# Performance work log

Measured on AMD Instinct MI355X. Metric: run time of the kernel, lower is better.

The kernel has to match this reference:

```python
import jax, jax.numpy as jnp
import numpy as np

NUM_BUSES = 20000
NUM_LINES = 320000
OTHER = 1000
BATCH = 128


def setup_inputs() -> dict:
    key = jax.random.key(0)
    k1, k2, k3, k4, k5 = jax.random.split(key, 5)
    x = jax.random.normal(k1, (BATCH, 2 * NUM_BUSES + OTHER), dtype=jnp.float32)
    from_indices = jax.random.randint(k2, (NUM_LINES,), 0, NUM_BUSES, dtype=jnp.int32)
    to_indices = jax.random.randint(k3, (NUM_LINES,), 0, NUM_BUSES, dtype=jnp.int32)
    # reactances bounded away from 0 (realistic p.u. line reactances)
    reactances = 0.01 + 0.2 * jax.random.uniform(k4, (NUM_LINES,), dtype=jnp.float32)
    limits = 0.5 + 1.5 * jax.random.uniform(k5, (NUM_LINES,), dtype=jnp.float32)
    return {
        "x": x,
        "from_indices": from_indices,
        "to_indices": to_indices,
        "reactances": reactances,
        "limits": limits,
        "num_buses": NUM_BUSES,
    }


def reference(x, from_indices, to_indices, reactances, limits, num_buses):
    nb = num_buses
    voltages = x[:, :nb]                     # [B, nb]
    angles = x[:, nb:2 * nb]                 # [B, nb]
    other_params = x[:, 2 * nb:]             # [B, other]

    from_a = angles[:, from_indices]         # [B, L] gather
    to_a = angles[:, to_indices]
    angle_diffs = from_a - to_a
    flows = angle_diffs / reactances[None, :]
    over = jnp.abs(flows / limits[None, :]) > 1.0

    # Torch runs this branch only if any line is over limit; when none are,
    # adjustments are identically zero, so applying unconditionally is exact.
    required = jnp.sign(angle_diffs) * (reactances * limits)[None, :]
    adjustments = jnp.where(over, required, angle_diffs) - angle_diffs  # [B, L]
    half = adjustments * 0.5
    # angles = angles + from_adjustments - to_adjustments
    #        = angles + scatter_add(from, adj/2) + scatter_add(to, adj/2)
    # (torch accumulates -adj/2 into to_adjustments, then subtracts it)
    delta = jnp.zeros_like(angles).at[:, from_indices].add(half).at[:, to_indices].add(half)
    angles2 = angles + delta

    diffs2 = angles2[:, from_indices] - angles2[:, to_indices]
    flows2 = diffs2 / reactances[None, :]

    out = jnp.concatenate([voltages, angles2, other_params], axis=1)
    return out, flows2
```

## Files before the change

kernel.cpp:

```cpp
#include <hip/hip_runtime.h>

#define NB     20000
#define NL     320000
#define NOTH   1000
#define BATCH  128
#define ROW    (2*NB + NOTH)
#define CAP    80
#define NBLK   256
#define LSEG   (NL/NBLK)
#define BCHUNK 8
#define CB     (NB/BCHUNK)
#define NSLICE 2
#define LPS    (NL/NSLICE)

__device__ __forceinline__ float fast_rcp(float a)
{
    float r;
    asm volatile("v_rcp_f32 %0, %1" : "=v"(r) : "v"(a));
    return r;
}

__global__ __launch_bounds__(512) void histo_k(
    const int* __restrict__ fidx, const int* __restrict__ tidx,
    ushort* __restrict__ H)
{
    extern __shared__ uint h[];
    for (int i = threadIdx.x; i < NB; i += 512) h[i] = 0u;
    __syncthreads();

    const int l0 = blockIdx.x * LSEG;
    for (int l = l0 + (int)threadIdx.x; l < l0 + LSEG; l += 512) {
        atomicAdd(&h[fidx[l]], 1u);
        atomicAdd(&h[tidx[l]], 1u);
    }
    __syncthreads();

    ushort* __restrict__ Hrow = H + (size_t)blockIdx.x * NB;
    for (int i = threadIdx.x; i < NB / 2; i += 512) {
        ushort2 u; u.x = (ushort)h[2 * i]; u.y = (ushort)h[2 * i + 1];
        ((ushort2*)Hrow)[i] = u;
    }
}

__global__ __launch_bounds__(512) void scan_k(
    ushort* __restrict__ H, int* __restrict__ cnt)
{
    const int u = blockIdx.x * 512 + threadIdx.x;
    if (u >= NB) return;
    uint run = 0;
    for (int b = 0; b < NBLK; ++b) {
        const uint v = H[(size_t)b * NB + u];
        H[(size_t)b * NB + u] = (ushort)run;
        run += v;
    }
    cnt[u] = (int)run;
}

__global__ __launch_bounds__(512) void place_k(
    const int* __restrict__ fidx, const int* __restrict__ tidx,
    const float* __restrict__ xr, const float* __restrict__ lim,
    const ushort* __restrict__ H, unsigned* __restrict__ bins)
{
    extern __shared__ char sm[];
    uint*   __restrict__ h    = (uint*)sm;
    ushort* __restrict__ pref = (ushort*)(sm + NB * 4);

    const ushort* __restrict__ Hrow = H + (size_t)blockIdx.x * NB;
    for (int i = threadIdx.x; i < NB; i += 512) h[i] = 0u;
    for (int i = threadIdx.x; i < NB / 2; i += 512)
        ((ushort2*)pref)[i] = ((const ushort2*)Hrow)[i];
    __syncthreads();

    const int l0 = blockIdx.x * LSEG;
    for (int l = l0 + (int)threadIdx.x; l < l0 + LSEG; l += 512) {
        const int fi = fidx[l];
        const int ti = tidx[l];
        union { float f; unsigned u; } c; c.f = xr[l] * lim[l];
        const unsigned rl16 = (c.u + 0x8000u) >> 16;

        const uint s0 = (uint)pref[fi] + atomicAdd(&h[fi], 1u);
        if (s0 < CAP) bins[(size_t)s0 * NB + fi] = ((unsigned)ti << 17) | rl16;
        const uint s1 = (uint)pref[ti] + atomicAdd(&h[ti], 1u);
        if (s1 < CAP) bins[(size_t)s1 * NB + ti] =
            ((unsigned)fi << 17) | (1u << 16) | rl16;
    }
}

__global__ __launch_bounds__(256) void zero_k(int* __restrict__ cnt)
{
    const int i = blockIdx.x * 256 + threadIdx.x;
    if (i < NB / 4) ((int4*)cnt)[i] = make_int4(0, 0, 0, 0);
}

__global__ __launch_bounds__(256) void build_k(
    const int* __restrict__ fidx, const int* __restrict__ tidx,
    const float* __restrict__ xr, const float* __restrict__ lim,
    int* __restrict__ cnt, unsigned* __restrict__ bins)
{
    const int q = blockIdx.x * 256 + threadIdx.x;
    if (q >= NL / 4) return;
    const int4   f = ((const int4*)fidx)[q];
    const int4   t = ((const int4*)tidx)[q];
    const float4 r = ((const float4*)xr)[q];
    const float4 L = ((const float4*)lim)[q];
    #define EMIT(FI, TI, RC, LC)                                             \
    {                                                                        \
        union { float f; unsigned u; } c; c.f = (RC) * (LC);                 \
        const unsigned rl16 = (c.u + 0x8000u) >> 16;                         \
        const int p0 = atomicAdd(&cnt[FI], 1);                               \
        if (p0 < CAP) bins[(size_t)p0 * NB + (FI)] =                         \
            ((unsigned)(TI) << 17) | rl16;                                   \
        const int p1 = atomicAdd(&cnt[TI], 1);                               \
        if (p1 < CAP) bins[(size_t)p1 * NB + (TI)] =                         \
            ((unsigned)(FI) << 17) | (1u << 16) | rl16;                      \
    }
    EMIT(f.x, t.x, r.x, L.x)
    EMIT(f.y, t.y, r.y, L.y)
    EMIT(f.z, t.z, r.z, L.z)
    EMIT(f.w, t.w, r.w, L.w)
    #undef EMIT
}

__global__ __launch_bounds__(1024) void delta_copy_k(
    const float* __restrict__ x, const int* __restrict__ cnt,
    const unsigned* __restrict__ bins, float* __restrict__ out)
{
    extern __shared__ float a[];
    const int b  = blockIdx.x % BATCH;
    const int cb = blockIdx.x / BATCH;

    const float* __restrict__ xrow = x   + (size_t)b * ROW;
    float*       __restrict__ orow = out + (size_t)b * ROW;

    for (int i = threadIdx.x; i < NB / 4; i += 1024)
        ((float4*)a)[i] = ((const float4*)(xrow + NB))[i];
    __syncthreads();

    for (int i = threadIdx.x; i < CB / 4; i += 1024)
        ((float4*)(orow + cb * CB))[i] = ((const float4*)(xrow + cb * CB))[i];
    if (cb == 0)
        for (int i = threadIdx.x; i < NOTH / 4; i += 1024)
            ((float4*)(orow + 2 * NB))[i] = ((const float4*)(xrow + 2 * NB))[i];

    const int base = cb * CB;
    for (int bus = base + (int)threadIdx.x; bus < base + CB; bus += 1024) {
        const int   n  = min(cnt[bus], CAP);
        const float ab = a[bus];
        float ds = 0.0f;
        int k = 0;
        #define CONTRIB(W)                                                   \
        {                                                                    \
            const unsigned w  = (W);                                         \
            const int   other = (int)(w >> 17);                              \
            const float rl    = __uint_as_float((w & 0xFFFFu) << 16);        \
            const float ad    = ab - a[other];                               \
            if (fabsf(ad) > rl) {                                            \
                float hh = 0.5f * (copysignf(rl, ad) - ad);                  \
                if (w & (1u << 16)) hh = -hh;                                \
                ds += hh;                                                    \
            }                                                                \
        }
        for (; k + 4 <= n; k += 4) {
            const unsigned w0 = bins[(size_t)(k + 0) * NB + bus];
            const unsigned w1 = bins[(size_t)(k + 1) * NB + bus];
            const unsigned w2 = bins[(size_t)(k + 2) * NB + bus];
            const unsigned w3 = bins[(size_t)(k + 3) * NB + bus];
            CONTRIB(w0) CONTRIB(w1) CONTRIB(w2) CONTRIB(w3)
        }
        for (; k < n; ++k) CONTRIB(bins[(size_t)k * NB + bus])
        #undef CONTRIB
        orow[NB + bus] = ab + ds;
    }
}

__global__ __launch_bounds__(1024) void flows_lds_k(
    const float* __restrict__ out, const int* __restrict__ fidx,
    const int* __restrict__ tidx, const float* __restrict__ xr,
    float* __restrict__ f2)
{
    extern __shared__ float a2[];
    const int b = blockIdx.x % BATCH;
    const int s = blockIdx.x / BATCH;

    const float* __restrict__ src = out + (size_t)b * ROW + NB;
    for (int i = threadIdx.x; i < NB / 4; i += 1024)
        ((float4*)a2)[i] = ((const float4*)src)[i];
    __syncthreads();

    float* __restrict__ frow = f2 + (size_t)b * NL;
    const int q0 = s * (LPS / 4);
    const int q1 = q0 + (LPS / 4);
    for (int q = q0 + (int)threadIdx.x; q < q1; q += 1024) {
        const int4   f = ((const int4*)fidx)[q];
        const int4   t = ((const int4*)tidx)[q];
        const float4 r = ((const float4*)xr)[q];
        float4 o;
        o.x = (a2[f.x] - a2[t.x]) * fast_rcp(r.x);
        o.y = (a2[f.y] - a2[t.y]) * fast_rcp(r.y);
        o.z = (a2[f.z] - a2[t.z]) * fast_rcp(r.z);
        o.w = (a2[f.w] - a2[t.w]) * fast_rcp(r.w);
        ((float4*)frow)[q] = o;
    }
}

extern "C" void kernel_launch(void* const* d_in, const int* in_sizes, int n_in,
                              void* d_out, int out_size, void* d_ws, size_t ws_size,
                              hipStream_t stream)
{
    const float* x   = (const float*)d_in[0];
    const int*   fi  = (const int*)  d_in[1];
    const int*   ti  = (const int*)  d_in[2];
    const float* xr  = (const float*)d_in[3];
    const float* lim = (const float*)d_in[4];

    float* out    = (float*)d_out;
    float* flows2 = out + (size_t)BATCH * ROW;

    const size_t hBytes = (size_t)NBLK * NB * sizeof(ushort);
    const size_t needed = hBytes + (size_t)NB * 4 + (size_t)CAP * NB * 4;

    int* cnt;
    unsigned* bins;

    if (ws_size >= needed) {
        ushort* H = (ushort*)d_ws;
        cnt  = (int*)((char*)d_ws + hBytes);
        bins = (unsigned*)((char*)d_ws + hBytes + (size_t)NB * 4);

        histo_k<<<dim3(NBLK), dim3(512), NB * sizeof(uint), stream>>>(fi, ti, H);
        scan_k<<<dim3((NB + 511) / 512), dim3(512), 0, stream>>>(H, cnt);
        place_k<<<dim3(NBLK), dim3(512),
                  NB * sizeof(uint) + NB * sizeof(ushort), stream>>>(
            fi, ti, xr, lim, H, bins);
    } else {
        cnt  = (int*)d_ws;
        bins = (unsigned*)((char*)d_ws + (size_t)NB * 4);
        zero_k<<<dim3((NB / 4 + 255) / 256), dim3(256), 0, stream>>>(cnt);
        build_k<<<dim3((NL / 4 + 255) / 256), dim3(256), 0, stream>>>(
            fi, ti, xr, lim, cnt, bins);
    }

    delta_copy_k<<<dim3(BCHUNK * BATCH), dim3(1024), NB * sizeof(float), stream>>>(
        x, cnt, bins, out);

    flows_lds_k<<<dim3(NSLICE * BATCH), dim3(1024), NB * sizeof(float), stream>>>(
        out, fi, ti, xr, flows2);
}
```

Baseline: 116.2 us.

## Overlap passthrough copy with scan, slice flows more, use nontemporal stores

Moves the voltage and other-params passthrough copy out of the delta kernel into extra blocks of the scan kernel. The scan uses only 40 blocks, so the idle CUs can do the copy alongside it. The flows kernel is split into 4 slices per batch row instead of 2 and writes its output with nontemporal stores. The workspace-size fallback path is removed, so the code now assumes the workspace is always large enough. Splitting into more slices means more blocks each reload the angle row into LDS.

```diff
diff --git a/kernel.cpp b/kernel.cpp
--- a/kernel.cpp
+++ b/kernel.cpp
@@ -10,8 +10,14 @@
 #define LSEG   (NL/NBLK)
 #define BCHUNK 8
 #define CB     (NB/BCHUNK)
-#define NSLICE 2
+#define NSLICE 4
 #define LPS    (NL/NSLICE)
+
+#define SCANB  40
+#define COPYB  256
+#define CPF4   (BATCH*(NB/4 + NOTH/4))
+
+typedef float vf4 __attribute__((ext_vector_type(4)));
 
 __device__ __forceinline__ float fast_rcp(float a)
 {
@@ -42,18 +48,31 @@
     }
 }
 
-__global__ __launch_bounds__(512) void scan_k(
-    ushort* __restrict__ H, int* __restrict__ cnt)
-{
-    const int u = blockIdx.x * 512 + threadIdx.x;
-    if (u >= NB) return;
-    uint run = 0;
-    for (int b = 0; b < NBLK; ++b) {
-        const uint v = H[(size_t)b * NB + u];
-        H[(size_t)b * NB + u] = (ushort)run;
-        run += v;
-    }
-    cnt[u] = (int)run;
+__global__ __launch_bounds__(512) void scancopy_k(
+    ushort* __restrict__ H, int* __restrict__ cnt,
+    const float* __restrict__ x, float* __restrict__ out)
+{
+    if (blockIdx.x < SCANB) {
+        const int u = blockIdx.x * 512 + threadIdx.x;
+        if (u >= NB) return;
+        uint run = 0;
+        for (int b = 0; b < NBLK; ++b) {
+            const uint v = H[(size_t)b * NB + u];
+            H[(size_t)b * NB + u] = (ushort)run;
+            run += v;
+        }
+        cnt[u] = (int)run;
+    } else {
+        const int nthr = COPYB * 512;
+        int idx = (blockIdx.x - SCANB) * 512 + threadIdx.x;
+        for (; idx < CPF4; idx += nthr) {
+            const int b = idx / (NB / 4 + NOTH / 4);
+            const int r = idx % (NB / 4 + NOTH / 4);
+            const int off = (r < NB / 4) ? r : (2 * NB / 4) + (r - NB / 4);
+            const size_t p = (size_t)b * (ROW / 4) + off;
+            ((float4*)out)[p] = ((const float4*)x)[p];
+        }
+    }
 }
 
 __global__ __launch_bounds__(512) void place_k(
@@ -86,42 +105,7 @@
     }
 }
 
-__global__ __launch_bounds__(256) void zero_k(int* __restrict__ cnt)
-{
-    const int i = blockIdx.x * 256 + threadIdx.x;
-    if (i < NB / 4) ((int4*)cnt)[i] = make_int4(0, 0, 0, 0);
-}
-
-__global__ __launch_bounds__(256) void build_k(
-    const int* __restrict__ fidx, const int* __restrict__ tidx,
-    const float* __restrict__ xr, const float* __restrict__ lim,
-    int* __restrict__ cnt, unsigned* __restrict__ bins)
-{
-    const int q = blockIdx.x * 256 + threadIdx.x;
-    if (q >= NL / 4) return;
-    const int4   f = ((const int4*)fidx)[q];
-    const int4   t = ((const int4*)tidx)[q];
-    const float4 r = ((const float4*)xr)[q];
-    const float4 L = ((const float4*)lim)[q];
-    #define EMIT(FI, TI, RC, LC)                                             \
-    {                                                                        \
-        union { float f; unsigned u; } c; c.f = (RC) * (LC);                 \
-        const unsigned rl16 = (c.u + 0x8000u) >> 16;                         \
-        const int p0 = atomicAdd(&cnt[FI], 1);                               \
-        if (p0 < CAP) bins[(size_t)p0 * NB + (FI)] =                         \
-            ((unsigned)(TI) << 17) | rl16;                                   \
-        const int p1 = atomicAdd(&cnt[TI], 1);                               \
-        if (p1 < CAP) bins[(size_t)p1 * NB + (TI)] =                         \
-            ((unsigned)(FI) << 17) | (1u << 16) | rl16;                      \
-    }
-    EMIT(f.x, t.x, r.x, L.x)
-    EMIT(f.y, t.y, r.y, L.y)
-    EMIT(f.z, t.z, r.z, L.z)
-    EMIT(f.w, t.w, r.w, L.w)
-    #undef EMIT
-}
-
-__global__ __launch_bounds__(1024) void delta_copy_k(
+__global__ __launch_bounds__(1024) void delta_k(
     const float* __restrict__ x, const int* __restrict__ cnt,
     const unsigned* __restrict__ bins, float* __restrict__ out)
 {
@@ -135,12 +119,6 @@
     for (int i = threadIdx.x; i < NB / 4; i += 1024)
         ((float4*)a)[i] = ((const float4*)(xrow + NB))[i];
     __syncthreads();
-
-    for (int i = threadIdx.x; i < CB / 4; i += 1024)
-        ((float4*)(orow + cb * CB))[i] = ((const float4*)(xrow + cb * CB))[i];
-    if (cb == 0)
-        for (int i = threadIdx.x; i < NOTH / 4; i += 1024)
-            ((float4*)(orow + 2 * NB))[i] = ((const float4*)(xrow + 2 * NB))[i];
 
     const int base = cb * CB;
     for (int bus = base + (int)threadIdx.x; bus < base + CB; bus += 1024) {
@@ -194,12 +172,12 @@
         const int4   f = ((const int4*)fidx)[q];
         const int4   t = ((const int4*)tidx)[q];
         const float4 r = ((const float4*)xr)[q];
-        float4 o;
+        vf4 o;
         o.x = (a2[f.x] - a2[t.x]) * fast_rcp(r.x);
         o.y = (a2[f.y] - a2[t.y]) * fast_rcp(r.y);
         o.z = (a2[f.z] - a2[t.z]) * fast_rcp(r.z);
         o.w = (a2[f.w] - a2[t.w]) * fast_rcp(r.w);
-        ((float4*)frow)[q] = o;
+        __builtin_nontemporal_store(o, &((vf4*)frow)[q]);
     }
 }
 
@@ -217,30 +195,19 @@
     float* flows2 = out + (size_t)BATCH * ROW;
 
     const size_t hBytes = (size_t)NBLK * NB * sizeof(ushort);
-    const size_t needed = hBytes + (size_t)NB * 4 + (size_t)CAP * NB * 4;
-
-    int* cnt;
-    unsigned* bins;
-
-    if (ws_size >= needed) {
-        ushort* H = (ushort*)d_ws;
-        cnt  = (int*)((char*)d_ws + hBytes);
-        bins = (unsigned*)((char*)d_ws + hBytes + (size_t)NB * 4);
-
-        histo_k<<<dim3(NBLK), dim3(512), NB * sizeof(uint), stream>>>(fi, ti, H);
-        scan_k<<<dim3((NB + 511) / 512), dim3(512), 0, stream>>>(H, cnt);
-        place_k<<<dim3(NBLK), dim3(512),
-                  NB * sizeof(uint) + NB * sizeof(ushort), stream>>>(
-            fi, ti, xr, lim, H, bins);
-    } else {
-        cnt  = (int*)d_ws;
-        bins = (unsigned*)((char*)d_ws + (size_t)NB * 4);
-        zero_k<<<dim3((NB / 4 + 255) / 256), dim3(256), 0, stream>>>(cnt);
-        build_k<<<dim3((NL / 4 + 255) / 256), dim3(256), 0, stream>>>(
-            fi, ti, xr, lim, cnt, bins);
-    }
-
-    delta_copy_k<<<dim3(BCHUNK * BATCH), dim3(1024), NB * sizeof(float), stream>>>(
+    ushort*   H    = (ushort*)d_ws;
+    int*      cnt  = (int*)((char*)d_ws + hBytes);
+    unsigned* bins = (unsigned*)((char*)d_ws + hBytes + (size_t)NB * 4);
+
+    histo_k<<<dim3(NBLK), dim3(512), NB * sizeof(uint), stream>>>(fi, ti, H);
+
+    scancopy_k<<<dim3(SCANB + COPYB), dim3(512), 0, stream>>>(H, cnt, x, out);
+
+    place_k<<<dim3(NBLK), dim3(512),
+              NB * sizeof(uint) + NB * sizeof(ushort), stream>>>(
+        fi, ti, xr, lim, H, bins);
+
+    delta_k<<<dim3(BCHUNK * BATCH), dim3(1024), NB * sizeof(float), stream>>>(
         x, cnt, bins, out);
 
     flows_lds_k<<<dim3(NSLICE * BATCH), dim3(1024), NB * sizeof(float), stream>>>(
```

After: 119.4 us. 2.8% more time.
